# Optimization experiments

Measured on AMD Instinct MI355X. Metric: run time of the kernel, lower is better.

The kernel has to match this reference:

```python
import jax, jax.numpy as jnp
import numpy as np


def setup_inputs() -> dict:
    key = jax.random.key(0)
    B, T = 1024, 16384
    n_b, n_a = 2, 2
    u_in = jax.random.normal(key, (B, T), dtype=jnp.float32)
    # initial conditions: y_init[:, i] = y[-1-i], u_init[:, i] = u[-1-i] (scipy lfiltic convention)
    y_init = jnp.zeros((B, n_a), dtype=jnp.float32)
    u_init = jnp.zeros((B, n_b), dtype=jnp.float32)
    # learnable transfer-function coefficients (stable 2nd-order system from the docstring)
    b_coeff = jnp.array([0.0, 0.0706464146944544], dtype=jnp.float32)
    a_coeff = jnp.array([-1.87212998940304, 0.942776404097492], dtype=jnp.float32)
    return {"b_coeff": b_coeff, "a_coeff": a_coeff, "u_in": u_in,
            "y_init": y_init, "u_init": u_init}


def _iir_filter(b_coeff, a_coeff, u_in, y_init, u_init):
    """y[t] = sum_{k=0}^{n_b-1} b_k u[t-k] - sum_{j=1}^{n_a} a_j y[t-j].

    Equivalent to scipy.signal.lfilter(b, [1, *a], u) with initial conditions.
    """
    B, T = u_in.shape
    n_b = b_coeff.shape[0]
    # prepend past inputs in chronological order: u_init[:, i] = u[-1-i]
    u_pad = jnp.concatenate([u_init[:, ::-1], u_in], axis=1)  # (B, n_b + T)
    # feedforward (FIR) part, fully vectorized over B and T
    x = jnp.zeros((B, T), dtype=u_in.dtype)
    for k in range(n_b):  # tiny fixed loop over filter taps
        x = x + b_coeff[k] * jax.lax.dynamic_slice_in_dim(u_pad, n_b - k, T, axis=1)

    # recurrent (IIR) part: carry last n_a outputs, newest first
    def step(yhist, x_t):
        y_t = x_t - yhist @ a_coeff          # (B,)
        yhist = jnp.concatenate([y_t[:, None], yhist[:, :-1]], axis=1)
        return yhist, y_t

    _, y = jax.lax.scan(step, y_init, x.T)   # scan over time; y: (T, B)
    return y.T


def reference(b_coeff, a_coeff, u_in, y_init, u_init):
    return _iir_filter(b_coeff, a_coeff, u_in, y_init, u_init)
```

## Files before the change

kernel.cpp:

```cpp
#include <hip/hip_runtime.h>


constexpr int T_LEN = 16384;
constexpr int LCH   = 64;
constexpr int NCH   = 256;

__global__ __launch_bounds__(NCH) void iir_kernel(
    const float* __restrict__ bco, const float* __restrict__ aco,
    const float* __restrict__ u,   const float* __restrict__ y_init,
    const float* __restrict__ u_init, float* __restrict__ y)
{
    __shared__ float sh_e1[NCH], sh_e2[NCH];
    __shared__ float sh_s1[NCH], sh_s2[NCH];

    const int row = blockIdx.x;
    const int tid = threadIdx.x;

    const float b0 = bco[0], b1 = bco[1];
    const float a1 = aco[0], a2 = aco[1];

    const float* __restrict__ urow = u + (size_t)row * T_LEN;
    float* __restrict__ yrow       = y + (size_t)row * T_LEN;
    const int base = tid * LCH;

    const float u_prev0 = (tid == 0) ? u_init[2 * row + 0] : urow[base - 1];

    const float4* __restrict__ u4 = (const float4*)(urow + base);

#define IIR_STEP(UC, OUTV)                                        \
    {                                                             \
        float x_ = fmaf(b0, (UC), b1 * up);                       \
        (OUTV) = fmaf(-a2, y2, fmaf(-a1, y1, x_));                \
        y2 = y1; y1 = (OUTV); up = (UC);                          \
    }

    float up = u_prev0, y1 = 0.f, y2 = 0.f;
    #pragma unroll
    for (int q = 0; q < LCH / 4; ++q) {
        float4 v = u4[q];
        float t0, t1c, t2c, t3c;
        IIR_STEP(v.x, t0);
        IIR_STEP(v.y, t1c);
        IIR_STEP(v.z, t2c);
        IIR_STEP(v.w, t3c);
        (void)t0; (void)t1c; (void)t2c; (void)t3c;
    }
    sh_e1[tid] = y1;
    sh_e2[tid] = y2;
    __syncthreads();

    if (tid == 0) {
        float pa = 1.f, pb = 0.f;
        #pragma unroll
        for (int k = 0; k <= LCH - 2; ++k) {
            float pn = fmaf(-a2, pb, -(a1 * pa));
            pb = pa; pa = pn;
        }
        const float pL2 = pa, pL3 = pb;
        const float pL1 = fmaf(-a2, pL3, -(a1 * pL2));
        const float qL1 = -a2 * pL2;
        const float qL2 = -a2 * pL3;

        float s1 = y_init[2 * row + 0];
        float s2 = y_init[2 * row + 1];
        for (int c = 0; c < NCH; ++c) {
            sh_s1[c] = s1; sh_s2[c] = s2;
            float n1 = fmaf(qL1, s2, fmaf(pL1, s1, sh_e1[c]));
            float n2 = fmaf(qL2, s2, fmaf(pL2, s1, sh_e2[c]));
            s1 = n1; s2 = n2;
        }
    }
    __syncthreads();

    up = u_prev0;
    y1 = sh_s1[tid];
    y2 = sh_s2[tid];
    float4* __restrict__ y4 = (float4*)(yrow + base);
    #pragma unroll
    for (int q = 0; q < LCH / 4; ++q) {
        float4 v = u4[q];
        float4 o;
        IIR_STEP(v.x, o.x);
        IIR_STEP(v.y, o.y);
        IIR_STEP(v.z, o.z);
        IIR_STEP(v.w, o.w);
        y4[q] = o;
    }
#undef IIR_STEP
}

extern "C" void kernel_launch(void* const* d_in, const int* in_sizes, int n_in,
                              void* d_out, int out_size, void* d_ws, size_t ws_size,
                              hipStream_t stream) {
    const float* b  = (const float*)d_in[0];
    const float* a  = (const float*)d_in[1];
    const float* u  = (const float*)d_in[2];
    const float* yi = (const float*)d_in[3];
    const float* ui = (const float*)d_in[4];
    float* yout = (float*)d_out;

    const int B = in_sizes[2] / T_LEN;
    iir_kernel<<<B, NCH, 0, stream>>>(b, a, u, yi, ui, yout);
}
```

Baseline: 149.8 us.

## Stage row through swizzled LDS for coalesced global loads and stores

Each block now loads its whole 64 KB row into shared memory with fully coalesced float4 accesses, using an XOR swizzle so that per-thread chunk reads avoid bank conflicts. Both IIR passes read from LDS instead of re-reading global memory with strided per-thread addresses. Outputs are written back into LDS in place and then stored to global memory coalesced. This removes the uncoalesced strided global traffic and the second read of the input. In exchange each block needs about 64 KB of LDS, which cuts occupancy to one or two blocks per CU and adds extra barriers.

```diff
diff --git a/kernel.cpp b/kernel.cpp
--- a/kernel.cpp
+++ b/kernel.cpp
@@ -5,11 +5,16 @@
 constexpr int LCH   = 64;
 constexpr int NCH   = 256;
 
+__device__ __forceinline__ int swz(int t, int q) {
+    return t * 16 + (q ^ (t & 15));
+}
+
 __global__ __launch_bounds__(NCH) void iir_kernel(
     const float* __restrict__ bco, const float* __restrict__ aco,
     const float* __restrict__ u,   const float* __restrict__ y_init,
     const float* __restrict__ u_init, float* __restrict__ y)
 {
+    __shared__ float4 lds[T_LEN / 4];
     __shared__ float sh_e1[NCH], sh_e2[NCH];
     __shared__ float sh_s1[NCH], sh_s2[NCH];
 
@@ -19,13 +24,24 @@
     const float b0 = bco[0], b1 = bco[1];
     const float a1 = aco[0], a2 = aco[1];
 
-    const float* __restrict__ urow = u + (size_t)row * T_LEN;
-    float* __restrict__ yrow       = y + (size_t)row * T_LEN;
-    const int base = tid * LCH;
+    const float4* __restrict__ u4 = (const float4*)(u + (size_t)row * T_LEN);
+    float4* __restrict__ y4       = (float4*)(y + (size_t)row * T_LEN);
 
-    const float u_prev0 = (tid == 0) ? u_init[2 * row + 0] : urow[base - 1];
+    #pragma unroll
+    for (int s = 0; s < 16; ++s) {
+        const int g = s * 256 + tid;
+        const int t = g >> 4, q = g & 15;
+        lds[swz(t, q)] = u4[g];
+    }
+    __syncthreads();
 
-    const float4* __restrict__ u4 = (const float4*)(urow + base);
+    float u_prev0;
+    if (tid == 0) {
+        u_prev0 = u_init[2 * row + 0];
+    } else {
+        const float* ldsf = (const float*)lds;
+        u_prev0 = ldsf[swz(tid - 1, 15) * 4 + 3];
+    }
 
 #define IIR_STEP(UC, OUTV)                                        \
     {                                                             \
@@ -36,8 +52,8 @@
 
     float up = u_prev0, y1 = 0.f, y2 = 0.f;
     #pragma unroll
-    for (int q = 0; q < LCH / 4; ++q) {
-        float4 v = u4[q];
+    for (int q = 0; q < 16; ++q) {
+        float4 v = lds[swz(tid, q)];
         float t0, t1c, t2c, t3c;
         IIR_STEP(v.x, t0);
         IIR_STEP(v.y, t1c);
@@ -75,18 +91,26 @@
     up = u_prev0;
     y1 = sh_s1[tid];
     y2 = sh_s2[tid];
-    float4* __restrict__ y4 = (float4*)(yrow + base);
     #pragma unroll
-    for (int q = 0; q < LCH / 4; ++q) {
-        float4 v = u4[q];
+    for (int q = 0; q < 16; ++q) {
+        const int slot = swz(tid, q);
+        float4 v = lds[slot];
         float4 o;
         IIR_STEP(v.x, o.x);
         IIR_STEP(v.y, o.y);
         IIR_STEP(v.z, o.z);
         IIR_STEP(v.w, o.w);
-        y4[q] = o;
+        lds[slot] = o;
     }
 #undef IIR_STEP
+    __syncthreads();
+
+    #pragma unroll
+    for (int s = 0; s < 16; ++s) {
+        const int g = s * 256 + tid;
+        const int t = g >> 4, q = g & 15;
+        y4[g] = lds[swz(t, q)];
+    }
 }
 
 extern "C" void kernel_launch(void* const* d_in, const int* in_sizes, int n_in,
```

After: 136.6 us. 8.8% less time.
